# Kernel tuning notes

Measured on AMD Instinct MI355X. Metric: run time of the kernel, lower is better.

The kernel has to match this reference:

```python
import jax, jax.numpy as jnp
import numpy as np

B, L, D, DF, E, R = 4, 1024, 1024, 4096, 32768, 64
EPS = 1e-6


def layer_norm(x, g, b, eps=EPS):
    mu = x.mean(-1, keepdims=True)
    var = ((x - mu) ** 2).mean(-1, keepdims=True)
    return (x - mu) * jax.lax.rsqrt(var + eps) * g + b


def setup_inputs() -> dict:
    key = jax.random.key(0)
    ks = jax.random.split(key, 16)
    s = 0.02
    return {
        "hidden_states": jax.random.normal(ks[0], (B, L, D), jnp.float32),
        "rel_table": jax.random.normal(ks[1], (R, D), jnp.float32) * s,
        "Wq": jax.random.normal(ks[2], (D, D), jnp.float32) * s,
        "bq": jnp.zeros((D,), jnp.float32),
        "Wk": jax.random.normal(ks[3], (D, D), jnp.float32) * s,
        "Wv": jax.random.normal(ks[4], (D, D), jnp.float32) * s,
        "Wo": jax.random.normal(ks[5], (D, D), jnp.float32) * s,
        "bo": jnp.zeros((D,), jnp.float32),
        "ln0_g": jnp.ones((D,), jnp.float32),
        "ln0_b": jnp.zeros((D,), jnp.float32),
        "ln1_g": jnp.ones((D,), jnp.float32),
        "ln1_b": jnp.zeros((D,), jnp.float32),
        "W1": jax.random.normal(ks[6], (D, DF), jnp.float32) * s,
        "b1": jnp.zeros((DF,), jnp.float32),
        "W2": jax.random.normal(ks[7], (DF, D), jnp.float32) * s,
        "b2": jnp.zeros((D,), jnp.float32),
        "ln2_g": jnp.ones((D,), jnp.float32),
        "ln2_b": jnp.zeros((D,), jnp.float32),
        "edge_src": jax.random.randint(ks[8], (B, E), 0, L, jnp.int32),
        "edge_dst": jax.random.randint(ks[9], (B, E), 0, L, jnp.int32),
        "edge_rel": jax.random.randint(ks[10], (B, E), 0, R, jnp.int32),
    }


def reference(hidden_states, rel_table, Wq, bq, Wk, Wv, Wo, bo,
              ln0_g, ln0_b, ln1_g, ln1_b, W1, b1, W2, b2, ln2_g, ln2_b,
              edge_src, edge_dst, edge_rel):
    scale = np.sqrt(D).astype(np.float32)  # num_heads=1 -> d_k = D
    hs_norm = layer_norm(hidden_states, ln0_g, ln0_b)

    def rgat_one(x, src, dst, rel):
        # x: [L, D]; src/dst/rel: [E]
        e = rel_table[rel]                       # [E, D] relation embeddings
        q = x @ Wq + bq
        k = x @ Wk
        v = x @ Wv
        score = jnp.sum((k[src] + e) * q[dst], axis=-1) / scale      # [E]
        score = jnp.exp(jnp.clip(score, -10.0, 10.0))
        wv = jax.ops.segment_sum((v[src] + e) * score[:, None], dst, num_segments=L)
        z = jax.ops.segment_sum(score, dst, num_segments=L)          # [L]
        o = wv / z[:, None]
        out = layer_norm(x + o @ Wo + bo, ln1_g, ln1_b)
        ffn = jnp.maximum(out @ W1 + b1, 0.0) @ W2 + b2
        return layer_norm(out + ffn, ln2_g, ln2_b)

    graph_rep = jax.vmap(rgat_one)(hs_norm, edge_src, edge_dst, edge_rel)
    out = jax.nn.elu(graph_rep)                  # dropout = identity (eval)
    return hidden_states + out
```

## Files before the change

### kernel.cpp

```cpp
#include <hip/hip_runtime.h>
#include <hip/hip_bf16.h>

#define B_SZ 4
#define L_SEQ 1024
#define D_MODEL 1024
#define DF_FF 4096
#define E_PER_B 32768
#define R_REL 64
#define M_ROWS (B_SZ * L_SEQ)

typedef __attribute__((ext_vector_type(8))) short bf16x8;
typedef __attribute__((ext_vector_type(4))) float f32x4;

__device__ inline float b2f(unsigned short u) {
    union { unsigned int i; float f; } x; x.i = ((unsigned int)u) << 16; return x.f;
}
__device__ inline unsigned short f2b(float f) {
    union { float f; unsigned int u; } x; x.f = f;
    unsigned int r = x.u + 0x7FFFu + ((x.u >> 16) & 1u);
    return (unsigned short)(r >> 16);
}

#define GLOBAL_CAST(p) ((const __attribute__((address_space(1))) void*)(p))
#define LDS_CAST(p)    ((__attribute__((address_space(3))) void*)(p))

#define LDB_WV 1088
#define BT_WV  (1024u * 1088u)
#define BT_QKV (1024u * 3072u)
#define SEXT_M 1152

__global__ void prep_all(const float* __restrict__ Wq, const float* __restrict__ Wk,
                         const float* __restrict__ Wv, const float* __restrict__ Wo,
                         const float* __restrict__ W1, const float* __restrict__ W2,
                         const float* __restrict__ rel, const float* __restrict__ bq,
                         const float* __restrict__ hidden,
                         const float* __restrict__ ln0_g, const float* __restrict__ ln0_b,
                         unsigned short* __restrict__ Wqkv_t, unsigned short* __restrict__ Wo_t,
                         unsigned short* __restrict__ W1_t, unsigned short* __restrict__ W2_t,
                         unsigned short* __restrict__ relbPad, unsigned short* __restrict__ Bwv,
                         float* __restrict__ bqkv,
                         unsigned short* __restrict__ Xn_b16,
                         float* __restrict__ zeroReg) {
    __shared__ float tile[32][33];
    __shared__ float sb1[4], sb2[4];
    const int id = blockIdx.x, tid = threadIdx.x;
    if (id < 12288) {
        const float* src; unsigned short* dst; int K, N, x, y;
        if (id < 4096) {
            const int seg = id >> 10, t = id & 1023;
            K = 1024; N = 1024; x = t & 31; y = t >> 5;
            src = (seg == 0) ? Wq : (seg == 1) ? Wk : (seg == 2) ? Wv : Wo;
            dst = (seg == 3) ? Wo_t : (Wqkv_t + (size_t)seg * 1048576);
        } else if (id < 8192) {
            const int t = id - 4096; K = 1024; N = 4096; x = t & 127; y = t >> 7;
            src = W1; dst = W1_t;
        } else {
            const int t = id - 8192; K = 4096; N = 1024; x = t & 31; y = t >> 5;
            src = W2; dst = W2_t;
        }
        const int n0 = x * 32, k0 = y * 32, tx = tid & 31, ty = tid >> 5;
#pragma unroll
        for (int r = 0; r < 32; r += 8)
            tile[ty + r][tx] = src[(size_t)(k0 + ty + r) * N + (n0 + tx)];
        __syncthreads();
#pragma unroll
        for (int r = 0; r < 32; r += 8)
            dst[(size_t)(n0 + ty + r) * K + (k0 + tx)] = f2b(tile[tx][ty + r]);
    } else if (id < 12800) {
        const int i = (id - 12288) * 256 + tid;
        relbPad[i] = (i < 65536) ? f2b(rel[i]) : (unsigned short)0;
    } else if (id < 13824) {
        const int i = (id - 12800) * 256 + tid;
        const int b = i >> 16, rem = i & 65535, d = rem >> 6, r = rem & 63;
        Bwv[(size_t)b * BT_WV + (size_t)d * LDB_WV + 1024 + r] = f2b(rel[r * 1024 + d]);
    } else if (id < 13836) {
        const int i = (id - 13824) * 256 + tid;
        bqkv[i] = (i < 1024) ? bq[i] : 0.0f;
    } else if (id < 17932) {
        const int row = id - 13836, t = tid;
        const size_t base = (size_t)row * 1024 + t * 4;
        float4 xv = *(const float4*)(hidden + base);
        float x0 = xv.x, x1 = xv.y, x2 = xv.z, x3 = xv.w;
        float s = x0 + x1 + x2 + x3;
#pragma unroll
        for (int o = 32; o > 0; o >>= 1) s += __shfl_down(s, o);
        if ((t & 63) == 0) sb1[t >> 6] = s;
        __syncthreads();
        const float mu = (sb1[0] + sb1[1] + sb1[2] + sb1[3]) * (1.0f / 1024.0f);
        const float d0 = x0 - mu, d1 = x1 - mu, d2 = x2 - mu, d3 = x3 - mu;
        float s2 = d0 * d0 + d1 * d1 + d2 * d2 + d3 * d3;
#pragma unroll
        for (int o = 32; o > 0; o >>= 1) s2 += __shfl_down(s2, o);
        if ((t & 63) == 0) sb2[t >> 6] = s2;
        __syncthreads();
        const float var = (sb2[0] + sb2[1] + sb2[2] + sb2[3]) * (1.0f / 1024.0f);
        const float rstd = rsqrtf(var + 1e-6f);
        const float4 gv = *(const float4*)(ln0_g + t * 4);
        const float4 bv = *(const float4*)(ln0_b + t * 4);
        ushort4 ob;
        ob.x = f2b(d0 * rstd * gv.x + bv.x);
        ob.y = f2b(d1 * rstd * gv.y + bv.y);
        ob.z = f2b(d2 * rstd * gv.z + bv.z);
        ob.w = f2b(d3 * rstd * gv.w + bv.w);
        *(ushort4*)(Xn_b16 + base) = ob;
    } else {
        const size_t base = (size_t)(id - 17932) * 4096 + tid * 4;
        const float4 z4 = make_float4(0.f, 0.f, 0.f, 0.f);
#pragma unroll
        for (int j = 0; j < 4; j++)
            *(float4*)(zeroReg + base + j * 1024) = z4;
    }
}

__device__ inline void tile_swizzle(int id, int ntn, int& tm, int& tn) {
    tm = ((id & 7) + ((id >> 3) / ntn) * 8) * 128;
    tn = ((id >> 3) % ntn) * 128;
}

template<bool OUT_BF16, bool RELU>
__global__ __launch_bounds__(256, 4)
void gemm_bf16(const unsigned short* __restrict__ A, int lda,
               const unsigned short* __restrict__ Bt, int ldb, size_t bt_batch,
               const float* __restrict__ bias,
               float* __restrict__ Cf, unsigned short* __restrict__ Cb,
               int N, int K, int ntn) {
    __shared__ unsigned short lA[128 * 64];
    __shared__ unsigned short lB[128 * 64];
    int tile_m, tile_n;
    tile_swizzle(blockIdx.x, ntn, tile_m, tile_n);
    const int t = threadIdx.x;
    const int wave = t >> 6, lane = t & 63;
    const int wm = (wave >> 1) * 64, wn = (wave & 1) * 64;
    const int quad = lane >> 4, l16 = lane & 15;

    const int srow = lane >> 3;
    const int schunk = ((lane & 7) ^ srow) * 8;
    const unsigned short* gA = A + (size_t)(tile_m + wave * 32 + srow) * lda + schunk;
    const unsigned short* gB = Bt + (size_t)(tile_m >> 10) * bt_batch
                                  + (size_t)(tile_n + wave * 32 + srow) * ldb + schunk;

    f32x4 acc[4][4];
#pragma unroll
    for (int i = 0; i < 4; i++)
#pragma unroll
        for (int j = 0; j < 4; j++) acc[i][j] = (f32x4)0.0f;

    for (int k0 = 0; k0 < K; k0 += 64) {
        __syncthreads();
#pragma unroll
        for (int r = 0; r < 4; ++r) {
            __builtin_amdgcn_global_load_lds(GLOBAL_CAST(gA + (size_t)r * 8 * lda),
                                             LDS_CAST(&lA[(wave * 32 + r * 8) * 64]), 16, 0, 0);
            __builtin_amdgcn_global_load_lds(GLOBAL_CAST(gB + (size_t)r * 8 * ldb),
                                             LDS_CAST(&lB[(wave * 32 + r * 8) * 64]), 16, 0, 0);
        }
        gA += 64; gB += 64;
        __builtin_amdgcn_s_waitcnt(0);
        __syncthreads();

#pragma unroll
        for (int kk = 0; kk < 2; ++kk) {
            const int cb = kk * 4 + quad;
            bf16x8 af[4], bf[4];
#pragma unroll
            for (int i = 0; i < 4; i++) {
                const int ra = wm + i * 16 + l16;
                af[i] = *(const bf16x8*)&lA[ra * 64 + ((cb ^ (ra & 7)) * 8)];
                const int rb = wn + i * 16 + l16;
                bf[i] = *(const bf16x8*)&lB[rb * 64 + ((cb ^ (rb & 7)) * 8)];
            }
#pragma unroll
            for (int mi = 0; mi < 4; mi++)
#pragma unroll
                for (int ni = 0; ni < 4; ni++)
                    acc[mi][ni] = __builtin_amdgcn_mfma_f32_16x16x32_bf16(af[mi], bf[ni], acc[mi][ni], 0, 0, 0);
        }
    }

#pragma unroll
    for (int mi = 0; mi < 4; mi++) {
#pragma unroll
        for (int ni = 0; ni < 4; ni++) {
            const int col = tile_n + wn + ni * 16 + l16;
            const float bv = bias[col];
#pragma unroll
            for (int r = 0; r < 4; r++) {
                const int row = tile_m + wm + mi * 16 + quad * 4 + r;
                float v = acc[mi][ni][r] + bv;
                if (RELU) v = fmaxf(v, 0.0f);
                if (OUT_BF16) Cb[(size_t)row * N + col] = f2b(v);
                else          Cf[(size_t)row * N + col] = v;
            }
        }
    }
}

__global__ __launch_bounds__(256, 4)
void gemm_bf16_splitk(const unsigned short* __restrict__ A, int lda,
                      const unsigned short* __restrict__ Bt, int ldb, size_t bt_batch,
                      const float* __restrict__ bias,
                      unsigned short* __restrict__ Pbase, size_t pstride,
                      int N, int Kc, int ntn) {
    __shared__ unsigned short lA[128 * 64];
    __shared__ unsigned short lB[128 * 64];
    int tile_m, tile_n;
    tile_swizzle(blockIdx.x, ntn, tile_m, tile_n);
    const int z = blockIdx.z;
    const int kofs = z * Kc;
    const int t = threadIdx.x;
    const int wave = t >> 6, lane = t & 63;
    const int wm = (wave >> 1) * 64, wn = (wave & 1) * 64;
    const int quad = lane >> 4, l16 = lane & 15;

    const int srow = lane >> 3;
    const int schunk = ((lane & 7) ^ srow) * 8;
    const unsigned short* gA = A + (size_t)(tile_m + wave * 32 + srow) * lda + kofs + schunk;
    const unsigned short* gB = Bt + (size_t)(tile_m >> 10) * bt_batch
                                  + (size_t)(tile_n + wave * 32 + srow) * ldb + kofs + schunk;

    f32x4 acc[4][4];
#pragma unroll
    for (int i = 0; i < 4; i++)
#pragma unroll
        for (int j = 0; j < 4; j++) acc[i][j] = (f32x4)0.0f;

    for (int k0 = 0; k0 < Kc; k0 += 64) {
        __syncthreads();
#pragma unroll
        for (int r = 0; r < 4; ++r) {
            __builtin_amdgcn_global_load_lds(GLOBAL_CAST(gA + (size_t)r * 8 * lda),
                                             LDS_CAST(&lA[(wave * 32 + r * 8) * 64]), 16, 0, 0);
            __builtin_amdgcn_global_load_lds(GLOBAL_CAST(gB + (size_t)r * 8 * ldb),
                                             LDS_CAST(&lB[(wave * 32 + r * 8) * 64]), 16, 0, 0);
        }
        gA += 64; gB += 64;
        __builtin_amdgcn_s_waitcnt(0);
        __syncthreads();

#pragma unroll
        for (int kk = 0; kk < 2; ++kk) {
            const int cb = kk * 4 + quad;
            bf16x8 af[4], bf[4];
#pragma unroll
            for (int i = 0; i < 4; i++) {
                const int ra = wm + i * 16 + l16;
                af[i] = *(const bf16x8*)&lA[ra * 64 + ((cb ^ (ra & 7)) * 8)];
                const int rb = wn + i * 16 + l16;
                bf[i] = *(const bf16x8*)&lB[rb * 64 + ((cb ^ (rb & 7)) * 8)];
            }
#pragma unroll
            for (int mi = 0; mi < 4; mi++)
#pragma unroll
                for (int ni = 0; ni < 4; ni++)
                    acc[mi][ni] = __builtin_amdgcn_mfma_f32_16x16x32_bf16(af[mi], bf[ni], acc[mi][ni], 0, 0, 0);
        }
    }

    unsigned short* P = Pbase + (size_t)z * pstride;
#pragma unroll
    for (int mi = 0; mi < 4; mi++) {
#pragma unroll
        for (int ni = 0; ni < 4; ni++) {
            const int col = tile_n + wn + ni * 16 + l16;
            const float bv = (z == 0) ? bias[col] : 0.0f;
#pragma unroll
            for (int r = 0; r < 4; r++) {
                const int row = tile_m + wm + mi * 16 + quad * 4 + r;
                P[(size_t)row * N + col] = f2b(acc[mi][ni][r] + bv);
            }
        }
    }
}

__global__ __launch_bounds__(256, 4)
void sext_tv(const unsigned short* __restrict__ QKV,
             const unsigned short* __restrict__ relPad,
             unsigned short* __restrict__ Pbase,
             unsigned short* __restrict__ Bwv, int Kc) {
    __shared__ unsigned short lA[128 * 64];
    __shared__ unsigned short lB[128 * 64];
    const int id = blockIdx.x, t = threadIdx.x;

    if (id >= 576) {
        unsigned short (*tile)[33] = (unsigned short (*)[33])lA;
        const int t2 = id - 576;
        const int b = t2 >> 10;
        const int d0 = (t2 & 31) * 32, s0 = ((t2 >> 5) & 31) * 32;
        const int tx = t & 31, ty = t >> 5;
#pragma unroll
        for (int r = 0; r < 32; r += 8)
            tile[ty + r][tx] = QKV[(size_t)((b << 10) + s0 + ty + r) * 3072 + 2048 + d0 + tx];
        __syncthreads();
#pragma unroll
        for (int r = 0; r < 32; r += 8)
            Bwv[(size_t)b * BT_WV + (size_t)(d0 + ty + r) * LDB_WV + s0 + tx] = tile[tx][ty + r];
        return;
    }

    const int bx = id % 72, b = (id / 72) & 3, z = id / 288;
    const int tile_m = (bx >> 3) * 128;
    const int tile_n = (bx & 7) * 128;
    const int kofs = z * Kc;
    const int wave = t >> 6, lane = t & 63;
    const int wm = (wave >> 1) * 64, wn = (wave & 1) * 64;
    const int quad = lane >> 4, l16 = lane & 15;

    const int srow = lane >> 3;
    const int schunk = ((lane & 7) ^ srow) * 8;
    const int arow = tile_m + wave * 32 + srow;
    const unsigned short* gA;
    size_t lda;
    if (tile_m < 1024) {
        gA = QKV + (size_t)b * BT_QKV + (size_t)arow * 3072 + 1024 + kofs + schunk;
        lda = 3072;
    } else {
        gA = relPad + (size_t)(arow - 1024) * 1024 + kofs + schunk;
        lda = 1024;
    }
    const unsigned short* gB = QKV + (size_t)b * BT_QKV
                                   + (size_t)(tile_n + wave * 32 + srow) * 3072 + kofs + schunk;

    f32x4 acc[4][4];
#pragma unroll
    for (int i = 0; i < 4; i++)
#pragma unroll
        for (int j = 0; j < 4; j++) acc[i][j] = (f32x4)0.0f;

    for (int k0 = 0; k0 < Kc; k0 += 64) {
        __syncthreads();
#pragma unroll
        for (int r = 0; r < 4; ++r) {
            __builtin_amdgcn_global_load_lds(GLOBAL_CAST(gA + (size_t)r * 8 * lda),
                                             LDS_CAST(&lA[(wave * 32 + r * 8) * 64]), 16, 0, 0);
            __builtin_amdgcn_global_load_lds(GLOBAL_CAST(gB + (size_t)r * 8 * 3072),
                                             LDS_CAST(&lB[(wave * 32 + r * 8) * 64]), 16, 0, 0);
        }
        gA += 64; gB += 64;
        __builtin_amdgcn_s_waitcnt(0);
        __syncthreads();

#pragma unroll
        for (int kk = 0; kk < 2; ++kk) {
            const int cb = kk * 4 + quad;
            bf16x8 af[4], bf[4];
#pragma unroll
            for (int i = 0; i < 4; i++) {
                const int ra = wm + i * 16 + l16;
                af[i] = *(const bf16x8*)&lA[ra * 64 + ((cb ^ (ra & 7)) * 8)];
                const int rb = wn + i * 16 + l16;
                bf[i] = *(const bf16x8*)&lB[rb * 64 + ((cb ^ (rb & 7)) * 8)];
            }
#pragma unroll
            for (int mi = 0; mi < 4; mi++)
#pragma unroll
                for (int ni = 0; ni < 4; ni++)
                    acc[mi][ni] = __builtin_amdgcn_mfma_f32_16x16x32_bf16(af[mi], bf[ni], acc[mi][ni], 0, 0, 0);
        }
    }

    unsigned short* P = Pbase + ((size_t)z * B_SZ + b) * (SEXT_M * 1024);
#pragma unroll
    for (int mi = 0; mi < 4; mi++) {
#pragma unroll
        for (int ni = 0; ni < 4; ni++) {
            const int col = tile_n + wn + ni * 16 + l16;
#pragma unroll
            for (int r = 0; r < 4; r++) {
                const int row = tile_m + wm + mi * 16 + quad * 4 + r;
                P[(size_t)row * 1024 + col] = f2b(acc[mi][ni][r]);
            }
        }
    }
}

template<bool FINAL, int NR>
__global__ void ln_kernel(const unsigned short* __restrict__ Xb,
                          const unsigned short* __restrict__ Rbase, size_t rstride,
                          const float* __restrict__ g, const float* __restrict__ be,
                          unsigned short* __restrict__ ob16,
                          const float* __restrict__ hidden, float* __restrict__ fout) {
    __shared__ float sb1[4], sb2[4];
    const int row = blockIdx.x, t = threadIdx.x;
    const size_t base = (size_t)row * 1024 + t * 4;

    ushort4 xv = *(const ushort4*)(Xb + base);
    float x0 = b2f(xv.x), x1 = b2f(xv.y), x2 = b2f(xv.z), x3 = b2f(xv.w);
#pragma unroll
    for (int r = 0; r < NR; r++) {
        ushort4 rv = *(const ushort4*)(Rbase + r * rstride + base);
        x0 += b2f(rv.x); x1 += b2f(rv.y); x2 += b2f(rv.z); x3 += b2f(rv.w);
    }
    float s = x0 + x1 + x2 + x3;
#pragma unroll
    for (int o = 32; o > 0; o >>= 1) s += __shfl_down(s, o);
    if ((t & 63) == 0) sb1[t >> 6] = s;
    __syncthreads();
    const float mu = (sb1[0] + sb1[1] + sb1[2] + sb1[3]) * (1.0f / 1024.0f);

    const float d0 = x0 - mu, d1 = x1 - mu, d2 = x2 - mu, d3 = x3 - mu;
    float s2 = d0 * d0 + d1 * d1 + d2 * d2 + d3 * d3;
#pragma unroll
    for (int o = 32; o > 0; o >>= 1) s2 += __shfl_down(s2, o);
    if ((t & 63) == 0) sb2[t >> 6] = s2;
    __syncthreads();
    const float var = (sb2[0] + sb2[1] + sb2[2] + sb2[3]) * (1.0f / 1024.0f);
    const float rstd = rsqrtf(var + 1e-6f);

    const float4 gv = *(const float4*)(g + t * 4);
    const float4 bv = *(const float4*)(be + t * 4);
    const float y0 = d0 * rstd * gv.x + bv.x;
    const float y1 = d1 * rstd * gv.y + bv.y;
    const float y2 = d2 * rstd * gv.z + bv.z;
    const float y3 = d3 * rstd * gv.w + bv.w;

    if (!FINAL) {
        ushort4 ob; ob.x = f2b(y0); ob.y = f2b(y1); ob.z = f2b(y2); ob.w = f2b(y3);
        *(ushort4*)(ob16 + base) = ob;
    } else {
        const float4 hv = *(const float4*)(hidden + base);
        const float e0 = y0 > 0.0f ? y0 : expm1f(y0);
        const float e1 = y1 > 0.0f ? y1 : expm1f(y1);
        const float e2 = y2 > 0.0f ? y2 : expm1f(y2);
        const float e3 = y3 > 0.0f ? y3 : expm1f(y3);
        float4 o; o.x = hv.x + e0; o.y = hv.y + e1; o.z = hv.z + e2; o.w = hv.w + e3;
        *(float4*)(fout + base) = o;
    }
}

__global__ void edge_scatter(const unsigned short* __restrict__ S,
                             const int* __restrict__ src, const int* __restrict__ dst,
                             const int* __restrict__ rel,
                             float* __restrict__ A, float* __restrict__ G) {
    const size_t ZSTR = (size_t)B_SZ * SEXT_M * 1024;
    const int gg = blockIdx.x * 256 + threadIdx.x;
    const int b = gg >> 15;
    const int s = src[gg], d = dst[gg], r = rel[gg];
    const size_t sbase = ((size_t)b * SEXT_M + s) * 1024 + d;
    const size_t tbase = ((size_t)b * SEXT_M + 1024 + r) * 1024 + d;
    const float sval = b2f(S[sbase]) + b2f(S[sbase + ZSTR]);
    const float tval = b2f(S[tbase]) + b2f(S[tbase + ZSTR]);
    float sc = (sval + tval) * (1.0f / 32.0f);
    sc = expf(fminf(fmaxf(sc, -10.0f), 10.0f));
    atomicAdd(&A[((size_t)((b << 10) + d) << 10) + s], sc);
    atomicAdd(&G[((size_t)((b << 10) + d) << 6) + r], sc);
}

__global__ void normalize(const float* __restrict__ A, const float* __restrict__ G,
                          unsigned short* __restrict__ Awv) {
    __shared__ float sInv;
    const int row = blockIdx.x, t = threadIdx.x;
    float v = 0.0f;
    if (t < 64) {
        v = G[(size_t)row * 64 + t];
        float s = v;
#pragma unroll
        for (int o = 1; o < 64; o <<= 1) s += __shfl_xor(s, o);
        if (t == 0) sInv = 1.0f / s;
    }
    __syncthreads();
    const float inv = sInv;
    const size_t obase = (size_t)row * LDB_WV;
    const float4 a = *(const float4*)(A + (size_t)row * 1024 + t * 4);
    ushort4 o;
    o.x = f2b(a.x * inv); o.y = f2b(a.y * inv); o.z = f2b(a.z * inv); o.w = f2b(a.w * inv);
    *(ushort4*)(Awv + obase + t * 4) = o;
    if (t < 16) {
        const float4 gq = *(const float4*)(G + (size_t)row * 64 + t * 4);
        ushort4 og;
        og.x = f2b(gq.x * inv); og.y = f2b(gq.y * inv);
        og.z = f2b(gq.z * inv); og.w = f2b(gq.w * inv);
        *(ushort4*)(Awv + obase + 1024 + t * 4) = og;
    }
}

extern "C" void kernel_launch(void* const* d_in, const int* in_sizes, int n_in,
                              void* d_out, int out_size, void* d_ws, size_t ws_size,
                              hipStream_t stream) {
    const float* hidden  = (const float*)d_in[0];
    const float* rel_tbl = (const float*)d_in[1];
    const float* Wq = (const float*)d_in[2];
    const float* bq = (const float*)d_in[3];
    const float* Wk = (const float*)d_in[4];
    const float* Wv = (const float*)d_in[5];
    const float* Wo = (const float*)d_in[6];
    const float* bo = (const float*)d_in[7];
    const float* ln0_g = (const float*)d_in[8];
    const float* ln0_b = (const float*)d_in[9];
    const float* ln1_g = (const float*)d_in[10];
    const float* ln1_b = (const float*)d_in[11];
    const float* W1 = (const float*)d_in[12];
    const float* b1 = (const float*)d_in[13];
    const float* W2 = (const float*)d_in[14];
    const float* b2 = (const float*)d_in[15];
    const float* ln2_g = (const float*)d_in[16];
    const float* ln2_b = (const float*)d_in[17];
    const int* esrc = (const int*)d_in[18];
    const int* edst = (const int*)d_in[19];
    const int* erel = (const int*)d_in[20];
    float* out = (float*)d_out;

    char* ws = (char*)d_ws;
    const size_t MB = 1024 * 1024;
    unsigned short* Xn_b16  = (unsigned short*)(ws + 16 * MB);
    unsigned short* H1      = (unsigned short*)(ws + 0);
    unsigned short* Wqkv_t  = (unsigned short*)(ws + 24 * MB);
    unsigned short* Wo_t    = (unsigned short*)(ws + 30 * MB);
    unsigned short* W1_t    = (unsigned short*)(ws + 32 * MB);
    unsigned short* W2_t    = (unsigned short*)(ws + 40 * MB);
    unsigned short* relbPad = (unsigned short*)(ws + 48 * MB);
    float*          bqkv    = (float*)(ws + 48 * MB + 512 * 1024);
    const float*    zbias   = bqkv + 1024;
    unsigned short* QKV     = (unsigned short*)(ws + 49 * MB);
    unsigned short* Awv     = (unsigned short*)(ws + 49 * MB);
    unsigned short* Obf     = (unsigned short*)(ws + 58 * MB);
    unsigned short* Qw2H    = (unsigned short*)(ws + 49 * MB);
    unsigned short* PwoH    = (unsigned short*)(ws + 66 * MB);
    unsigned short* SxH     = (unsigned short*)(ws + 73 * MB);
    unsigned short* Bwv     = (unsigned short*)(ws + 92 * MB);
    float*          Amat    = (float*)(ws + 101 * MB);
    float*          Gmat    = (float*)(ws + 117 * MB);
    unsigned short* Out_b16 = (unsigned short*)(ws + 113 * MB);

    const size_t PSTRIDE_H = 4u * 1024 * 1024;
    const dim3 blk(256);

    prep_all<<<19020, blk, 0, stream>>>(Wq, Wk, Wv, Wo, W1, W2, rel_tbl, bq,
                                        hidden, ln0_g, ln0_b,
                                        Wqkv_t, Wo_t, W1_t, W2_t, relbPad, Bwv, bqkv,
                                        Xn_b16, Amat);
    gemm_bf16<true, false><<<dim3(24 * 32), blk, 0, stream>>>(
        Xn_b16, 1024, Wqkv_t, 1024, 0, bqkv, nullptr, QKV, 3072, 1024, 24);
    sext_tv<<<4672, blk, 0, stream>>>(QKV, relbPad, SxH, Bwv, 512);
    edge_scatter<<<512, blk, 0, stream>>>(SxH, esrc, edst, erel, Amat, Gmat);
    normalize<<<M_ROWS, blk, 0, stream>>>(Amat, Gmat, Awv);
    gemm_bf16<true, false><<<dim3(8 * 32), blk, 0, stream>>>(
        Awv, LDB_WV, Bwv, LDB_WV, BT_WV, zbias, nullptr, Obf, 1024, LDB_WV, 8);
    gemm_bf16_splitk<<<dim3(8 * 32, 1, 2), blk, 0, stream>>>(
        Obf, 1024, Wo_t, 1024, 0, bo, PwoH, PSTRIDE_H, 1024, 512, 8);
    ln_kernel<false, 2><<<M_ROWS, blk, 0, stream>>>(Xn_b16, PwoH, PSTRIDE_H, ln1_g, ln1_b,
                                                    Out_b16, nullptr, nullptr);
    gemm_bf16<true, true><<<dim3(32 * 32), blk, 0, stream>>>(
        Out_b16, 1024, W1_t, 1024, 0, b1, nullptr, H1, 4096, 1024, 32);
    gemm_bf16_splitk<<<dim3(8 * 32, 1, 4), blk, 0, stream>>>(
        H1, 4096, W2_t, 4096, 0, b2, Qw2H, PSTRIDE_H, 1024, 1024, 8);
    ln_kernel<true, 4><<<M_ROWS, blk, 0, stream>>>(Out_b16, Qw2H, PSTRIDE_H, ln2_g, ln2_b,
                                                   nullptr, hidden, out);
    (void)in_sizes; (void)n_in; (void)out_size; (void)ws_size;
}
```

Measured before the change: 363.3 us.

## Fold Wo into V and relation table to skip separate Wo GEMM

Precomputes the per-batch product of Wo with the transposed V values and relation embeddings inside the score-extension kernel, then does one split-K GEMM of the normalized aggregate against this combined matrix. This replaces the aggregate@V GEMM followed by a separate Wo GEMM and removes the V transpose pass. In exchange it adds an extra 1024x1152x1024 GEMM per batch, and rounds the fused weight to bf16, which could change accuracy slightly. The GEMM inner loop is also factored into a shared macro.

```diff
diff --git a/kernel.cpp b/kernel.cpp
--- a/kernel.cpp
+++ b/kernel.cpp
@@ -24,10 +24,11 @@
 #define GLOBAL_CAST(p) ((const __attribute__((address_space(1))) void*)(p))
 #define LDS_CAST(p)    ((__attribute__((address_space(3))) void*)(p))
 
-#define LDB_WV 1088
-#define BT_WV  (1024u * 1088u)
 #define BT_QKV (1024u * 3072u)
 #define SEXT_M 1152
+#define LDA_WV 1088
+#define LDB_WVP 1152
+#define BT_WVP (1024u * 1152u)
 
 __global__ void prep_all(const float* __restrict__ Wq, const float* __restrict__ Wk,
                          const float* __restrict__ Wv, const float* __restrict__ Wo,
@@ -37,7 +38,7 @@
                          const float* __restrict__ ln0_g, const float* __restrict__ ln0_b,
                          unsigned short* __restrict__ Wqkv_t, unsigned short* __restrict__ Wo_t,
                          unsigned short* __restrict__ W1_t, unsigned short* __restrict__ W2_t,
-                         unsigned short* __restrict__ relbPad, unsigned short* __restrict__ Bwv,
+                         unsigned short* __restrict__ relbPad,
                          float* __restrict__ bqkv,
                          unsigned short* __restrict__ Xn_b16,
                          float* __restrict__ zeroReg) {
@@ -69,15 +70,11 @@
     } else if (id < 12800) {
         const int i = (id - 12288) * 256 + tid;
         relbPad[i] = (i < 65536) ? f2b(rel[i]) : (unsigned short)0;
-    } else if (id < 13824) {
+    } else if (id < 12812) {
         const int i = (id - 12800) * 256 + tid;
-        const int b = i >> 16, rem = i & 65535, d = rem >> 6, r = rem & 63;
-        Bwv[(size_t)b * BT_WV + (size_t)d * LDB_WV + 1024 + r] = f2b(rel[r * 1024 + d]);
-    } else if (id < 13836) {
-        const int i = (id - 13824) * 256 + tid;
         bqkv[i] = (i < 1024) ? bq[i] : 0.0f;
-    } else if (id < 17932) {
-        const int row = id - 13836, t = tid;
+    } else if (id < 16908) {
+        const int row = id - 12812, t = tid;
         const size_t base = (size_t)row * 1024 + t * 4;
         float4 xv = *(const float4*)(hidden + base);
         float x0 = xv.x, x1 = xv.y, x2 = xv.z, x3 = xv.w;
@@ -104,7 +101,7 @@
         ob.w = f2b(d3 * rstd * gv.w + bv.w);
         *(ushort4*)(Xn_b16 + base) = ob;
     } else {
-        const size_t base = (size_t)(id - 17932) * 4096 + tid * 4;
+        const size_t base = (size_t)(id - 16908) * 4096 + tid * 4;
         const float4 z4 = make_float4(0.f, 0.f, 0.f, 0.f);
 #pragma unroll
         for (int j = 0; j < 4; j++)
@@ -116,6 +113,37 @@
     tm = ((id & 7) + ((id >> 3) / ntn) * 8) * 128;
     tn = ((id >> 3) % ntn) * 128;
 }
+
+#define GEMM_BODY(GA, LDA_, GB, LDB_, KLEN)                                                 \
+    f32x4 acc[4][4];                                                                        \
+    _Pragma("unroll") for (int i = 0; i < 4; i++)                                           \
+        _Pragma("unroll") for (int j = 0; j < 4; j++) acc[i][j] = (f32x4)0.0f;              \
+    for (int k0 = 0; k0 < (KLEN); k0 += 64) {                                               \
+        __syncthreads();                                                                    \
+        _Pragma("unroll") for (int r = 0; r < 4; ++r) {                                     \
+            __builtin_amdgcn_global_load_lds(GLOBAL_CAST((GA) + (size_t)r * 8 * (LDA_)),    \
+                LDS_CAST(&lA[(wave * 32 + r * 8) * 64]), 16, 0, 0);                         \
+            __builtin_amdgcn_global_load_lds(GLOBAL_CAST((GB) + (size_t)r * 8 * (LDB_)),    \
+                LDS_CAST(&lB[(wave * 32 + r * 8) * 64]), 16, 0, 0);                         \
+        }                                                                                   \
+        (GA) += 64; (GB) += 64;                                                             \
+        __builtin_amdgcn_s_waitcnt(0);                                                      \
+        __syncthreads();                                                                    \
+        _Pragma("unroll") for (int kk = 0; kk < 2; ++kk) {                                  \
+            const int cb = kk * 4 + quad;                                                   \
+            bf16x8 af[4], bf[4];                                                            \
+            _Pragma("unroll") for (int i = 0; i < 4; i++) {                                 \
+                const int ra = wm + i * 16 + l16;                                           \
+                af[i] = *(const bf16x8*)&lA[ra * 64 + ((cb ^ (ra & 7)) * 8)];               \
+                const int rb = wn + i * 16 + l16;                                           \
+                bf[i] = *(const bf16x8*)&lB[rb * 64 + ((cb ^ (rb & 7)) * 8)];               \
+            }                                                                               \
+            _Pragma("unroll") for (int mi = 0; mi < 4; mi++)                                \
+                _Pragma("unroll") for (int ni = 0; ni < 4; ni++)                            \
+                    acc[mi][ni] = __builtin_amdgcn_mfma_f32_16x16x32_bf16(                  \
+                        af[mi], bf[ni], acc[mi][ni], 0, 0, 0);                              \
+        }                                                                                   \
+    }
 
 template<bool OUT_BF16, bool RELU>
 __global__ __launch_bounds__(256, 4)
@@ -132,51 +160,12 @@
     const int wave = t >> 6, lane = t & 63;
     const int wm = (wave >> 1) * 64, wn = (wave & 1) * 64;
     const int quad = lane >> 4, l16 = lane & 15;
-
     const int srow = lane >> 3;
     const int schunk = ((lane & 7) ^ srow) * 8;
     const unsigned short* gA = A + (size_t)(tile_m + wave * 32 + srow) * lda + schunk;
     const unsigned short* gB = Bt + (size_t)(tile_m >> 10) * bt_batch
                                   + (size_t)(tile_n + wave * 32 + srow) * ldb + schunk;
-
-    f32x4 acc[4][4];
-#pragma unroll
-    for (int i = 0; i < 4; i++)
-#pragma unroll
-        for (int j = 0; j < 4; j++) acc[i][j] = (f32x4)0.0f;
-
-    for (int k0 = 0; k0 < K; k0 += 64) {
-        __syncthreads();
-#pragma unroll
-        for (int r = 0; r < 4; ++r) {
-            __builtin_amdgcn_global_load_lds(GLOBAL_CAST(gA + (size_t)r * 8 * lda),
-                                             LDS_CAST(&lA[(wave * 32 + r * 8) * 64]), 16, 0, 0);
-            __builtin_amdgcn_global_load_lds(GLOBAL_CAST(gB + (size_t)r * 8 * ldb),
-                                             LDS_CAST(&lB[(wave * 32 + r * 8) * 64]), 16, 0, 0);
-        }
-        gA += 64; gB += 64;
-        __builtin_amdgcn_s_waitcnt(0);
-        __syncthreads();
-
-#pragma unroll
-        for (int kk = 0; kk < 2; ++kk) {
-            const int cb = kk * 4 + quad;
-            bf16x8 af[4], bf[4];
-#pragma unroll
-            for (int i = 0; i < 4; i++) {
-                const int ra = wm + i * 16 + l16;
-                af[i] = *(const bf16x8*)&lA[ra * 64 + ((cb ^ (ra & 7)) * 8)];
-                const int rb = wn + i * 16 + l16;
-                bf[i] = *(const bf16x8*)&lB[rb * 64 + ((cb ^ (rb & 7)) * 8)];
-            }
-#pragma unroll
-            for (int mi = 0; mi < 4; mi++)
-#pragma unroll
-                for (int ni = 0; ni < 4; ni++)
-                    acc[mi][ni] = __builtin_amdgcn_mfma_f32_16x16x32_bf16(af[mi], bf[ni], acc[mi][ni], 0, 0, 0);
-        }
-    }
-
+    GEMM_BODY(gA, lda, gB, ldb, K)
 #pragma unroll
     for (int mi = 0; mi < 4; mi++) {
 #pragma unroll
@@ -211,51 +200,12 @@
     const int wave = t >> 6, lane = t & 63;
     const int wm = (wave >> 1) * 64, wn = (wave & 1) * 64;
     const int quad = lane >> 4, l16 = lane & 15;
-
     const int srow = lane >> 3;
     const int schunk = ((lane & 7) ^ srow) * 8;
     const unsigned short* gA = A + (size_t)(tile_m + wave * 32 + srow) * lda + kofs + schunk;
     const unsigned short* gB = Bt + (size_t)(tile_m >> 10) * bt_batch
                                   + (size_t)(tile_n + wave * 32 + srow) * ldb + kofs + schunk;
-
-    f32x4 acc[4][4];
-#pragma unroll
-    for (int i = 0; i < 4; i++)
-#pragma unroll
-        for (int j = 0; j < 4; j++) acc[i][j] = (f32x4)0.0f;
-
-    for (int k0 = 0; k0 < Kc; k0 += 64) {
-        __syncthreads();
-#pragma unroll
-        for (int r = 0; r < 4; ++r) {
-            __builtin_amdgcn_global_load_lds(GLOBAL_CAST(gA + (size_t)r * 8 * lda),
-                                             LDS_CAST(&lA[(wave * 32 + r * 8) * 64]), 16, 0, 0);
-            __builtin_amdgcn_global_load_lds(GLOBAL_CAST(gB + (size_t)r * 8 * ldb),
-                                             LDS_CAST(&lB[(wave * 32 + r * 8) * 64]), 16, 0, 0);
-        }
-        gA += 64; gB += 64;
-        __builtin_amdgcn_s_waitcnt(0);
-        __syncthreads();
-
-#pragma unroll
-        for (int kk = 0; kk < 2; ++kk) {
-            const int cb = kk * 4 + quad;
-            bf16x8 af[4], bf[4];
-#pragma unroll
-            for (int i = 0; i < 4; i++) {
-                const int ra = wm + i * 16 + l16;
-                af[i] = *(const bf16x8*)&lA[ra * 64 + ((cb ^ (ra & 7)) * 8)];
-                const int rb = wn + i * 16 + l16;
-                bf[i] = *(const bf16x8*)&lB[rb * 64 + ((cb ^ (rb & 7)) * 8)];
-            }
-#pragma unroll
-            for (int mi = 0; mi < 4; mi++)
-#pragma unroll
-                for (int ni = 0; ni < 4; ni++)
-                    acc[mi][ni] = __builtin_amdgcn_mfma_f32_16x16x32_bf16(af[mi], bf[ni], acc[mi][ni], 0, 0, 0);
-        }
-    }
-
+    GEMM_BODY(gA, lda, gB, ldb, Kc)
     unsigned short* P = Pbase + (size_t)z * pstride;
 #pragma unroll
     for (int mi = 0; mi < 4; mi++) {
@@ -273,27 +223,50 @@
 }
 
 __global__ __launch_bounds__(256, 4)
-void sext_tv(const unsigned short* __restrict__ QKV,
-             const unsigned short* __restrict__ relPad,
-             unsigned short* __restrict__ Pbase,
-             unsigned short* __restrict__ Bwv, int Kc) {
+void sext_w(const unsigned short* __restrict__ QKV,
+            const unsigned short* __restrict__ relPad,
+            const unsigned short* __restrict__ Wo_t,
+            unsigned short* __restrict__ Pbase,
+            unsigned short* __restrict__ Bwvp, int Kc) {
     __shared__ unsigned short lA[128 * 64];
     __shared__ unsigned short lB[128 * 64];
     const int id = blockIdx.x, t = threadIdx.x;
+    const int wave = t >> 6, lane = t & 63;
+    const int wm = (wave >> 1) * 64, wn = (wave & 1) * 64;
+    const int quad = lane >> 4, l16 = lane & 15;
+    const int srow = lane >> 3;
+    const int schunk = ((lane & 7) ^ srow) * 8;
 
     if (id >= 576) {
-        unsigned short (*tile)[33] = (unsigned short (*)[33])lA;
         const int t2 = id - 576;
-        const int b = t2 >> 10;
-        const int d0 = (t2 & 31) * 32, s0 = ((t2 >> 5) & 31) * 32;
-        const int tx = t & 31, ty = t >> 5;
-#pragma unroll
-        for (int r = 0; r < 32; r += 8)
-            tile[ty + r][tx] = QKV[(size_t)((b << 10) + s0 + ty + r) * 3072 + 2048 + d0 + tx];
-        __syncthreads();
-#pragma unroll
-        for (int r = 0; r < 32; r += 8)
-            Bwv[(size_t)b * BT_WV + (size_t)(d0 + ty + r) * LDB_WV + s0 + tx] = tile[tx][ty + r];
+        const int b = t2 / 72, rem = t2 % 72;
+        const int tile_m = (rem / 9) * 128;
+        const int tile_n = (rem % 9) * 128;
+        const unsigned short* gA = Wo_t + (size_t)(tile_m + wave * 32 + srow) * 1024 + schunk;
+        const int brow = tile_n + wave * 32 + srow;
+        const unsigned short* gB;
+        size_t ldb;
+        if (tile_n < 1024) {
+            gB = QKV + (size_t)b * BT_QKV + (size_t)brow * 3072 + 2048 + schunk;
+            ldb = 3072;
+        } else {
+            gB = relPad + (size_t)(brow - 1024) * 1024 + schunk;
+            ldb = 1024;
+        }
+        GEMM_BODY(gA, 1024, gB, ldb, 1024)
+        unsigned short* P = Bwvp + (size_t)b * BT_WVP;
+#pragma unroll
+        for (int mi = 0; mi < 4; mi++) {
+#pragma unroll
+            for (int ni = 0; ni < 4; ni++) {
+                const int col = tile_n + wn + ni * 16 + l16;
+#pragma unroll
+                for (int r = 0; r < 4; r++) {
+                    const int row = tile_m + wm + mi * 16 + quad * 4 + r;
+                    P[(size_t)row * LDB_WVP + col] = f2b(acc[mi][ni][r]);
+                }
+            }
+        }
         return;
     }
 
@@ -301,12 +274,6 @@
     const int tile_m = (bx >> 3) * 128;
     const int tile_n = (bx & 7) * 128;
     const int kofs = z * Kc;
-    const int wave = t >> 6, lane = t & 63;
-    const int wm = (wave >> 1) * 64, wn = (wave & 1) * 64;
-    const int quad = lane >> 4, l16 = lane & 15;
-
-    const int srow = lane >> 3;
-    const int schunk = ((lane & 7) ^ srow) * 8;
     const int arow = tile_m + wave * 32 + srow;
     const unsigned short* gA;
     size_t lda;
@@ -319,45 +286,7 @@
     }
     const unsigned short* gB = QKV + (size_t)b * BT_QKV
                                    + (size_t)(tile_n + wave * 32 + srow) * 3072 + kofs + schunk;
-
-    f32x4 acc[4][4];
-#pragma unroll
-    for (int i = 0; i < 4; i++)
-#pragma unroll
-        for (int j = 0; j < 4; j++) acc[i][j] = (f32x4)0.0f;
-
-    for (int k0 = 0; k0 < Kc; k0 += 64) {
-        __syncthreads();
-#pragma unroll
-        for (int r = 0; r < 4; ++r) {
-            __builtin_amdgcn_global_load_lds(GLOBAL_CAST(gA + (size_t)r * 8 * lda),
-                                             LDS_CAST(&lA[(wave * 32 + r * 8) * 64]), 16, 0, 0);
-            __builtin_amdgcn_global_load_lds(GLOBAL_CAST(gB + (size_t)r * 8 * 3072),
-                                             LDS_CAST(&lB[(wave * 32 + r * 8) * 64]), 16, 0, 0);
-        }
-        gA += 64; gB += 64;
-        __builtin_amdgcn_s_waitcnt(0);
-        __syncthreads();
-
-#pragma unroll
-        for (int kk = 0; kk < 2; ++kk) {
-            const int cb = kk * 4 + quad;
-            bf16x8 af[4], bf[4];
-#pragma unroll
-            for (int i = 0; i < 4; i++) {
-                const int ra = wm + i * 16 + l16;
-                af[i] = *(const bf16x8*)&lA[ra * 64 + ((cb ^ (ra & 7)) * 8)];
-                const int rb = wn + i * 16 + l16;
-                bf[i] = *(const bf16x8*)&lB[rb * 64 + ((cb ^ (rb & 7)) * 8)];
-            }
-#pragma unroll
-            for (int mi = 0; mi < 4; mi++)
-#pragma unroll
-                for (int ni = 0; ni < 4; ni++)
-                    acc[mi][ni] = __builtin_amdgcn_mfma_f32_16x16x32_bf16(af[mi], bf[ni], acc[mi][ni], 0, 0, 0);
-        }
-    }
-
+    GEMM_BODY(gA, lda, gB, 3072, Kc)
     unsigned short* P = Pbase + ((size_t)z * B_SZ + b) * (SEXT_M * 1024);
 #pragma unroll
     for (int mi = 0; mi < 4; mi++) {
@@ -368,6 +297,44 @@
             for (int r = 0; r < 4; r++) {
                 const int row = tile_m + wm + mi * 16 + quad * 4 + r;
                 P[(size_t)row * 1024 + col] = f2b(acc[mi][ni][r]);
+            }
+        }
+    }
+}
+
+__global__ __launch_bounds__(256, 4)
+void gemm_wv_splitk(const unsigned short* __restrict__ A,
+                    const unsigned short* __restrict__ Bt,
+                    const float* __restrict__ bias,
+                    unsigned short* __restrict__ Pbase, size_t pstride) {
+    __shared__ unsigned short lA[128 * 64];
+    __shared__ unsigned short lB[128 * 64];
+    int tile_m, tile_n;
+    tile_swizzle(blockIdx.x, 8, tile_m, tile_n);
+    const int z = blockIdx.z;
+    const int kofs = z * 576;
+    const int Kc = z ? 512 : 576;
+    const int t = threadIdx.x;
+    const int wave = t >> 6, lane = t & 63;
+    const int wm = (wave >> 1) * 64, wn = (wave & 1) * 64;
+    const int quad = lane >> 4, l16 = lane & 15;
+    const int srow = lane >> 3;
+    const int schunk = ((lane & 7) ^ srow) * 8;
+    const unsigned short* gA = A + (size_t)(tile_m + wave * 32 + srow) * LDA_WV + kofs + schunk;
+    const unsigned short* gB = Bt + (size_t)(tile_m >> 10) * BT_WVP
+                                  + (size_t)(tile_n + wave * 32 + srow) * LDB_WVP + kofs + schunk;
+    GEMM_BODY(gA, LDA_WV, gB, LDB_WVP, Kc)
+    unsigned short* P = Pbase + (size_t)z * pstride;
+#pragma unroll
+    for (int mi = 0; mi < 4; mi++) {
+#pragma unroll
+        for (int ni = 0; ni < 4; ni++) {
+            const int col = tile_n + wn + ni * 16 + l16;
+            const float bv = (z == 0) ? bias[col] : 0.0f;
+#pragma unroll
+            for (int r = 0; r < 4; r++) {
+                const int row = tile_m + wm + mi * 16 + quad * 4 + r;
+                P[(size_t)row * 1024 + col] = f2b(acc[mi][ni][r] + bv);
             }
         }
     }
@@ -459,7 +426,7 @@
     }
     __syncthreads();
     const float inv = sInv;
-    const size_t obase = (size_t)row * LDB_WV;
+    const size_t obase = (size_t)row * LDA_WV;
     const float4 a = *(const float4*)(A + (size_t)row * 1024 + t * 4);
     ushort4 o;
     o.x = f2b(a.x * inv); o.y = f2b(a.y * inv); o.z = f2b(a.z * inv); o.w = f2b(a.w * inv);
@@ -509,14 +476,12 @@
     unsigned short* W2_t    = (unsigned short*)(ws + 40 * MB);
     unsigned short* relbPad = (unsigned short*)(ws + 48 * MB);
     float*          bqkv    = (float*)(ws + 48 * MB + 512 * 1024);
-    const float*    zbias   = bqkv + 1024;
     unsigned short* QKV     = (unsigned short*)(ws + 49 * MB);
     unsigned short* Awv     = (unsigned short*)(ws + 49 * MB);
-    unsigned short* Obf     = (unsigned short*)(ws + 58 * MB);
     unsigned short* Qw2H    = (unsigned short*)(ws + 49 * MB);
     unsigned short* PwoH    = (unsigned short*)(ws + 66 * MB);
     unsigned short* SxH     = (unsigned short*)(ws + 73 * MB);
-    unsigned short* Bwv     = (unsigned short*)(ws + 92 * MB);
+    unsigned short* Bwvp    = (unsigned short*)(ws + 92 * MB);
     float*          Amat    = (float*)(ws + 101 * MB);
     float*          Gmat    = (float*)(ws + 117 * MB);
     unsigned short* Out_b16 = (unsigned short*)(ws + 113 * MB);
@@ -524,19 +489,16 @@
     const size_t PSTRIDE_H = 4u * 1024 * 1024;
     const dim3 blk(256);
 
-    prep_all<<<19020, blk, 0, stream>>>(Wq, Wk, Wv, Wo, W1, W2, rel_tbl, bq,
+    prep_all<<<17996, blk, 0, stream>>>(Wq, Wk, Wv, Wo, W1, W2, rel_tbl, bq,
                                         hidden, ln0_g, ln0_b,
-                                        Wqkv_t, Wo_t, W1_t, W2_t, relbPad, Bwv, bqkv,
+                                        Wqkv_t, Wo_t, W1_t, W2_t, relbPad, bqkv,
                                         Xn_b16, Amat);
     gemm_bf16<true, false><<<dim3(24 * 32), blk, 0, stream>>>(
         Xn_b16, 1024, Wqkv_t, 1024, 0, bqkv, nullptr, QKV, 3072, 1024, 24);
-    sext_tv<<<4672, blk, 0, stream>>>(QKV, relbPad, SxH, Bwv, 512);
+    sext_w<<<864, blk, 0, stream>>>(QKV, relbPad, Wo_t, SxH, Bwvp, 512);
     edge_scatter<<<512, blk, 0, stream>>>(SxH, esrc, edst, erel, Amat, Gmat);
     normalize<<<M_ROWS, blk, 0, stream>>>(Amat, Gmat, Awv);
-    gemm_bf16<true, false><<<dim3(8 * 32), blk, 0, stream>>>(
-        Awv, LDB_WV, Bwv, LDB_WV, BT_WV, zbias, nullptr, Obf, 1024, LDB_WV, 8);
-    gemm_bf16_splitk<<<dim3(8 * 32, 1, 2), blk, 0, stream>>>(
-        Obf, 1024, Wo_t, 1024, 0, bo, PwoH, PSTRIDE_H, 1024, 512, 8);
+    gemm_wv_splitk<<<dim3(256, 1, 2), blk, 0, stream>>>(Awv, Bwvp, bo, PwoH, PSTRIDE_H);
     ln_kernel<false, 2><<<M_ROWS, blk, 0, stream>>>(Xn_b16, PwoH, PSTRIDE_H, ln1_g, ln1_b,
                                                     Out_b16, nullptr, nullptr);
     gemm_bf16<true, true><<<dim3(32 * 32), blk, 0, stream>>>(
```

New measurement: 352.1 us. 1.03x faster.
